# Performance work log

Measured on AMD Instinct MI355X. Metric: run time of the kernel, lower is better.

Reference implementation:

```python
import jax, jax.numpy as jnp
import numpy as np
import math

TAU = 0.04
BIG = 100000.0


def _decay(initial, step, steps):
    de = initial * 0.75 * (1.0 + math.cos(math.pi * step / (steps / 2.0)))
    dm = initial * 0.75 * (1.0 + math.cos(math.pi * step / steps))
    e = de if step < steps / 2.0 else 0.0
    m = dm
    return e, m, 3.0 - e - m


def _normalize(x):
    return x / jnp.maximum(jnp.linalg.norm(x, axis=1, keepdims=True), 1e-12)


def _pdist(a2, b2, ab):
    # ||a_i||^2 + ||b_j||^2 - 2 a_i.b_j, clamped + sqrt (matches torch addmm_ path)
    return jnp.sqrt(jnp.clip(a2 + b2.T - 2.0 * ab, 1e-12, None))


def _row_extreme(masked, is_min):
    idx = jnp.argmin(masked, axis=1) if is_min else jnp.argmax(masked, axis=1)
    val = jnp.take_along_axis(masked, idx[:, None], axis=1)[:, 0]
    return val, idx


def _nanmedian(vals, mask):
    # lower-median over valid entries per row (torch.nanmedian semantics)
    k = mask.sum(axis=1)
    pos = jnp.maximum((k - 1) // 2, 0)
    order = jnp.argsort(jnp.where(mask, vals, jnp.inf), axis=1)
    med_idx = jnp.take_along_axis(order, pos[:, None], axis=1)[:, 0]
    med_val = jnp.take_along_axis(vals, med_idx[:, None], axis=1)[:, 0]
    med_val = jnp.where(k > 0, med_val, 0.0)  # NaN-median -> 0 as in source
    return med_val, med_idx


def _ce0(logits):
    # CrossEntropy with labels all 0 over 2 classes
    return jnp.mean(jax.nn.logsumexp(logits, axis=1) - logits[:, 0])


def _pair_loss(dist_vals_an, dist_vals_ap, an_t, ap_t):
    sg = jax.lax.stop_gradient
    w_an = jnp.clip(sg(an_t) - sg(dist_vals_an), 0.0, None)
    w_ap = jnp.clip(sg(dist_vals_ap) - sg(ap_t), 0.0, None)
    logits = jnp.stack([w_an * dist_vals_an / TAU, w_ap * dist_vals_ap / TAU], axis=1)
    return _ce0(logits)


def _forward(teacher_inputs, inputs, epoch):
    e, m, d = _decay(0.5, epoch, 240)
    t = _normalize(teacher_inputs)
    s = _normalize(inputs)
    t2 = jnp.sum(t * t, axis=1, keepdims=True)  # [n,1]
    s2 = jnp.sum(s * s, axis=1, keepdims=True)
    dist_t = _pdist(t2, t2, t @ t.T)            # teacher-teacher [n,n]
    dist = _pdist(t2, s2, t @ s.T)              # teacher-student [n,n]
    temp1 = jnp.diag(dist)[:, None]             # dist[i,i] broadcast over row i
    neg_mask = dist_t > temp1
    pos_mask = ~neg_mask

    gather_t = lambda idx: jnp.take_along_axis(dist_t, idx[:, None], axis=1)[:, 0]

    # hard mining (d-branch): nearest negative, farthest positive
    an_v, an_i = _row_extreme(jnp.where(neg_mask, dist, BIG), True)
    ap_v, ap_i = _row_extreme(jnp.where(pos_mask, dist, 0.0), False)
    loss_d = _pair_loss(an_v, ap_v, gather_t(an_i), gather_t(ap_i))

    # easy mining (e-branch): farthest negative, nearest positive
    an_ev, an_ei = _row_extreme(jnp.where(neg_mask, dist, 0.0), False)
    ap_ev, ap_ei = _row_extreme(jnp.where(pos_mask, dist, BIG), True)
    loss_e = _pair_loss(an_ev, ap_ev, gather_t(an_ei), gather_t(ap_ei))

    # median mining (m-branch)
    an_mv, an_mi = _nanmedian(dist, neg_mask)
    ap_mv, ap_mi = _nanmedian(dist, pos_mask)
    loss_m = _pair_loss(an_mv, ap_mv, gather_t(an_mi), gather_t(ap_mi))

    return loss_e * e + loss_m * m + loss_d * d


def setup_inputs() -> dict:
    key = jax.random.key(0)
    k1, k2 = jax.random.split(key)
    n, dim = 4096, 2048
    return {
        "teacher_inputs": jax.random.normal(k1, (n, dim), dtype=jnp.float32),
        "inputs": jax.random.normal(k2, (n, dim), dtype=jnp.float32),
        "epoch": 100,
    }


def reference(teacher_inputs, inputs, epoch):
    return _forward(teacher_inputs, inputs, epoch)
```

## Files before the change

### kernel.cpp

```cpp
#include <hip/hip_runtime.h>
#include <math.h>
#include <cfloat>
#include <climits>

#define NROW 4096
#define DIM  2048
#define BIGF 100000.0f
#define BIGU 0x47C35000u

typedef float  f32x4  __attribute__((ext_vector_type(4)));
typedef __bf16 bf16x8 __attribute__((ext_vector_type(8)));
typedef unsigned short us8v __attribute__((ext_vector_type(8)));

__device__ __forceinline__ unsigned short f2bf(float x) {
    unsigned u = __float_as_uint(x);
    u += 0x7fffu + ((u >> 16) & 1u);
    return (unsigned short)(u >> 16);
}
__device__ __forceinline__ float bf2f(unsigned short h) {
    return __uint_as_float(((unsigned)h) << 16);
}

__device__ __forceinline__ void gload16(const void* g, void* lds) {
    __builtin_amdgcn_global_load_lds(
        (const __attribute__((address_space(1))) unsigned int*)g,
        (__attribute__((address_space(3))) unsigned int*)lds,
        16, 0, 0);
}

__global__ __launch_bounds__(256) void k_norm_split(const float* __restrict__ in,
    unsigned short* __restrict__ hi, unsigned short* __restrict__ lo,
    float* __restrict__ sq)
{
    int row = blockIdx.x;
    int tid = threadIdx.x;
    const float4* rp = (const float4*)(in + (size_t)row * DIM);
    float4 v0 = rp[tid * 2 + 0];
    float4 v1 = rp[tid * 2 + 1];
    float ss = v0.x*v0.x + v0.y*v0.y + v0.z*v0.z + v0.w*v0.w
             + v1.x*v1.x + v1.y*v1.y + v1.z*v1.z + v1.w*v1.w;
    #pragma unroll
    for (int off = 32; off > 0; off >>= 1) ss += __shfl_down(ss, off, 64);
    __shared__ float wsum[4];
    __shared__ float s_den;
    if ((tid & 63) == 0) wsum[tid >> 6] = ss;
    __syncthreads();
    if (tid == 0) {
        float tot = wsum[0] + wsum[1] + wsum[2] + wsum[3];
        float den = fmaxf(sqrtf(tot), 1e-12f);
        s_den = den;
        sq[row] = tot / (den * den);
    }
    __syncthreads();
    float den = s_den;
    float xs[8];
    xs[0]=v0.x/den; xs[1]=v0.y/den; xs[2]=v0.z/den; xs[3]=v0.w/den;
    xs[4]=v1.x/den; xs[5]=v1.y/den; xs[6]=v1.z/den; xs[7]=v1.w/den;
    us8v hv, lv;
    #pragma unroll
    for (int j = 0; j < 8; ++j) {
        unsigned short h = f2bf(xs[j]);
        hv[j] = h;
        lv[j] = f2bf(xs[j] - bf2f(h));
    }
    *(us8v*)&hi[(size_t)row * DIM + tid * 8] = hv;
    *(us8v*)&lo[(size_t)row * DIM + tid * 8] = lv;
}

__global__ __launch_bounds__(256, 2) void k_gemm_mfma(
    const unsigned short* __restrict__ T1, const unsigned short* __restrict__ T2,
    const unsigned short* __restrict__ S1, const unsigned short* __restrict__ S2,
    const float* __restrict__ t2v, const float* __restrict__ s2v,
    float* __restrict__ distT, float* __restrict__ distS)
{
    __shared__ unsigned short As[128 * 32];
    __shared__ unsigned short Bt[128 * 32];
    __shared__ unsigned short Bs[128 * 32];

    int tid = threadIdx.x;

    int orig  = blockIdx.y * gridDim.x + blockIdx.x;
    int nwg   = gridDim.x * gridDim.y;
    int cpx   = nwg >> 3;
    int swz   = (orig & 7) * cpx + (orig >> 3);
    int bx    = swz % gridDim.x;
    int by    = swz / gridDim.x;
    int m0 = by * 128, n0 = bx * 128;

    int r0   = tid >> 2;
    int cs0  = (((tid & 3) ^ ((r0 >> 1) & 3)) << 4);
    unsigned ldst = (unsigned)tid * 16;

    int l  = tid & 63;
    int w  = tid >> 6;
    int wr = w >> 1, wc = w & 1;
    int lr = l & 15;
    int kc = l >> 4;

    f32x4 acc_t[4][4], acc_s[4][4];
    #pragma unroll
    for (int m = 0; m < 4; ++m)
        #pragma unroll
        for (int n = 0; n < 4; ++n) {
            acc_t[m][n] = (f32x4)0.0f;
            acc_s[m][n] = (f32x4)0.0f;
        }

    const unsigned short* segA[3]  = {T1, T1, T2};
    const unsigned short* segBt[3] = {T1, T2, T1};
    const unsigned short* segBs[3] = {S1, S2, S1};

    for (int seg = 0; seg < 3; ++seg) {
        const char* pA  = (const char*)segA[seg];
        const char* pBt = (const char*)segBt[seg];
        const char* pBs = (const char*)segBs[seg];
        for (int k0 = 0; k0 < DIM; k0 += 32) {
            size_t gA0 = ((size_t)(m0 + r0)      * DIM + k0) * 2 + cs0;
            size_t gA1 = ((size_t)(m0 + 64 + r0) * DIM + k0) * 2 + cs0;
            size_t gB0 = ((size_t)(n0 + r0)      * DIM + k0) * 2 + cs0;
            size_t gB1 = ((size_t)(n0 + 64 + r0) * DIM + k0) * 2 + cs0;
            gload16(pA  + gA0, (char*)As + ldst);
            gload16(pA  + gA1, (char*)As + 4096 + ldst);
            gload16(pBt + gB0, (char*)Bt + ldst);
            gload16(pBt + gB1, (char*)Bt + 4096 + ldst);
            gload16(pBs + gB0, (char*)Bs + ldst);
            gload16(pBs + gB1, (char*)Bs + 4096 + ldst);
            __syncthreads();

            bf16x8 a[4], btf[4], bsf[4];
            #pragma unroll
            for (int m = 0; m < 4; ++m) {
                int ra = wr * 64 + m * 16 + lr;
                int co = ((kc ^ ((ra >> 1) & 3)) << 4);
                a[m] = *(const bf16x8*)((const char*)As + ra * 64 + co);
            }
            #pragma unroll
            for (int n = 0; n < 4; ++n) {
                int rb = wc * 64 + n * 16 + lr;
                int co = ((kc ^ ((rb >> 1) & 3)) << 4);
                btf[n] = *(const bf16x8*)((const char*)Bt + rb * 64 + co);
                bsf[n] = *(const bf16x8*)((const char*)Bs + rb * 64 + co);
            }
            #pragma unroll
            for (int m = 0; m < 4; ++m)
                #pragma unroll
                for (int n = 0; n < 4; ++n) {
                    acc_t[m][n] = __builtin_amdgcn_mfma_f32_16x16x32_bf16(
                        a[m], btf[n], acc_t[m][n], 0, 0, 0);
                    acc_s[m][n] = __builtin_amdgcn_mfma_f32_16x16x32_bf16(
                        a[m], bsf[n], acc_s[m][n], 0, 0, 0);
                }
            __syncthreads();
        }
    }

    int colb = n0 + wc * 64 + lr;
    int rowb = m0 + wr * 64 + (kc << 2);
    float t2row[4][4];
    #pragma unroll
    for (int m = 0; m < 4; ++m)
        #pragma unroll
        for (int r = 0; r < 4; ++r) t2row[m][r] = t2v[rowb + m * 16 + r];
    #pragma unroll
    for (int n = 0; n < 4; ++n) {
        int col = colb + n * 16;
        float t2c = t2v[col];
        float s2c = s2v[col];
        #pragma unroll
        for (int m = 0; m < 4; ++m) {
            f32x4 ct = acc_t[m][n];
            f32x4 cs = acc_s[m][n];
            int row = rowb + m * 16;
            #pragma unroll
            for (int r = 0; r < 4; ++r) {
                size_t o = (size_t)(row + r) * NROW + col;
                distT[o] = sqrtf(fmaxf(t2row[m][r] + t2c - 2.0f * ct[r], 1e-12f));
                distS[o] = sqrtf(fmaxf(t2row[m][r] + s2c - 2.0f * cs[r], 1e-12f));
            }
        }
    }
}

__device__ inline float pair_term(float an_v, float ap_v, float an_t, float ap_t)
{
    float w_an = fmaxf(an_t - an_v, 0.f);
    float w_ap = fmaxf(ap_v - ap_t, 0.f);
    float l0 = w_an * an_v / 0.04f;
    float l1 = w_ap * ap_v / 0.04f;
    float mx = fmaxf(l0, l1);
    return mx + logf(expf(l0 - mx) + expf(l1 - mx)) - l0;
}

__device__ __forceinline__ unsigned long long wred_min64(unsigned long long v) {
    #pragma unroll
    for (int o = 32; o > 0; o >>= 1) {
        unsigned long long x = __shfl_down(v, o, 64);
        v = (x < v) ? x : v;
    }
    return v;
}
__device__ __forceinline__ unsigned long long wred_max64(unsigned long long v) {
    #pragma unroll
    for (int o = 32; o > 0; o >>= 1) {
        unsigned long long x = __shfl_down(v, o, 64);
        v = (x > v) ? x : v;
    }
    return v;
}

__device__ void radix_select_reg(const unsigned u[16], unsigned negbits,
                                 unsigned selNeg, int rank,
                                 unsigned* hist, unsigned* s_wt, unsigned* s_sel,
                                 int tid, float& val, int& idx)
{
    unsigned prefix = 0;
    int r = rank;
    #pragma unroll
    for (int pass = 0; pass < 4; ++pass) {
        const int shift = 24 - pass * 8;
        hist[tid] = 0;
        __syncthreads();
        {
            unsigned curbin = 0xFFFFFFFFu, rl = 0;
            #pragma unroll
            for (int q = 0; q < 16; ++q) {
                unsigned key = (((negbits >> q) & 1u) == selNeg) ? u[q] : 0xFFFFFFFFu;
                bool match = (pass == 0) || ((key >> (shift + 8)) == (prefix >> (shift + 8)));
                if (match) {
                    unsigned b = (key >> shift) & 255u;
                    if (b == curbin) { rl++; }
                    else {
                        if (rl) atomicAdd(&hist[curbin], rl);
                        curbin = b; rl = 1;
                    }
                }
            }
            if (rl) atomicAdd(&hist[curbin], rl);
        }
        __syncthreads();
        unsigned h = hist[tid];
        unsigned incl = h;
        #pragma unroll
        for (int o = 1; o < 64; o <<= 1) {
            unsigned x = __shfl_up(incl, o, 64);
            if ((tid & 63) >= o) incl += x;
        }
        if ((tid & 63) == 63) s_wt[tid >> 6] = incl;
        __syncthreads();
        int wv = tid >> 6;
        unsigned base = 0;
        if (wv > 0) base += s_wt[0];
        if (wv > 1) base += s_wt[1];
        if (wv > 2) base += s_wt[2];
        incl += base;
        unsigned excl = incl - h;
        if ((unsigned)r >= excl && (unsigned)r < incl) {
            s_sel[0] = (unsigned)tid;
            s_sel[1] = (unsigned)r - excl;
        }
        __syncthreads();
        prefix |= s_sel[0] << shift;
        r = (int)s_sel[1];
        __syncthreads();
    }
    {
        unsigned cnt = 0;
        #pragma unroll
        for (int q = 0; q < 16; ++q) {
            unsigned key = (((negbits >> q) & 1u) == selNeg) ? u[q] : 0xFFFFFFFFu;
            if (key == prefix) cnt++;
        }
        hist[tid] = cnt;
        __syncthreads();
        unsigned incl = hist[tid];
        #pragma unroll
        for (int o = 1; o < 64; o <<= 1) {
            unsigned x = __shfl_up(incl, o, 64);
            if ((tid & 63) >= o) incl += x;
        }
        if ((tid & 63) == 63) s_wt[tid >> 6] = incl;
        __syncthreads();
        int wv = tid >> 6;
        unsigned base = 0;
        if (wv > 0) base += s_wt[0];
        if (wv > 1) base += s_wt[1];
        if (wv > 2) base += s_wt[2];
        incl += base;
        unsigned excl = incl - cnt;
        if ((unsigned)r >= excl && (unsigned)r < incl) {
            int need = r - (int)excl;
            #pragma unroll
            for (int q = 0; q < 16; ++q) {
                unsigned key = (((negbits >> q) & 1u) == selNeg) ? u[q] : 0xFFFFFFFFu;
                if (key == prefix) {
                    if (need == 0) { s_sel[0] = (unsigned)(tid * 16 + q); }
                    need--;
                }
            }
        }
        __syncthreads();
    }
    val = __uint_as_float(prefix);
    idx = (int)s_sel[0];
    __syncthreads();
}

__global__ __launch_bounds__(256) void k_rowstats(const float* __restrict__ distS,
    const float* __restrict__ distT, float* __restrict__ terms)
{
    __shared__ unsigned hist[256];
    __shared__ unsigned s_wt[4];
    __shared__ unsigned s_sel[2];
    __shared__ unsigned long long s_red[4][4];
    __shared__ int s_cw[4];
    __shared__ float s_t1;

    int i = blockIdx.x, tid = threadIdx.x;
    const float* dSrow = distS + (size_t)i * NROW;
    const float* dTrow = distT + (size_t)i * NROW;

    if (tid == 0) s_t1 = dSrow[i];

    float4 dv[4], tv[4];
    #pragma unroll
    for (int c = 0; c < 4; ++c) {
        dv[c] = *(const float4*)(dSrow + tid * 16 + c * 4);
        tv[c] = *(const float4*)(dTrow + tid * 16 + c * 4);
    }
    __syncthreads();
    float temp1 = s_t1;

    unsigned u[16];
    unsigned negbits = 0;
    #pragma unroll
    for (int c = 0; c < 4; ++c) {
        const float* dp = (const float*)&dv[c];
        const float* tp = (const float*)&tv[c];
        #pragma unroll
        for (int k = 0; k < 4; ++k) {
            int q = c * 4 + k;
            u[q] = __float_as_uint(dp[k]);
            if (tp[k] > temp1) negbits |= (1u << q);
        }
    }

    unsigned long long Pan  = ~0ull;
    unsigned long long Pap  = 0ull;
    unsigned long long Pane = 0ull;
    unsigned long long Pape = ~0ull;
    int cnt = 0;
    #pragma unroll
    for (int q = 0; q < 16; ++q) {
        unsigned j = (unsigned)(tid * 16 + q);
        unsigned neg = (negbits >> q) & 1u;
        cnt += (int)neg;
        unsigned kan  = neg ? u[q] : BIGU;
        unsigned kap  = neg ? 0u   : u[q];
        unsigned kane = neg ? u[q] : 0u;
        unsigned kape = neg ? BIGU : u[q];
        unsigned long long pan  = ((unsigned long long)kan  << 32) | j;
        unsigned long long pap  = ((unsigned long long)kap  << 32) | (0xFFFFFFFFu - j);
        unsigned long long pane = ((unsigned long long)kane << 32) | (0xFFFFFFFFu - j);
        unsigned long long pape = ((unsigned long long)kape << 32) | j;
        if (pan  < Pan)  Pan  = pan;
        if (pap  > Pap)  Pap  = pap;
        if (pane > Pane) Pane = pane;
        if (pape < Pape) Pape = pape;
    }
    Pan  = wred_min64(Pan);
    Pap  = wred_max64(Pap);
    Pane = wred_max64(Pane);
    Pape = wred_min64(Pape);
    #pragma unroll
    for (int o = 32; o > 0; o >>= 1) cnt += __shfl_down(cnt, o, 64);
    if ((tid & 63) == 0) {
        int wv = tid >> 6;
        s_red[0][wv] = Pan; s_red[1][wv] = Pap;
        s_red[2][wv] = Pane; s_red[3][wv] = Pape;
        s_cw[wv] = cnt;
    }
    __syncthreads();
    unsigned long long Ran = ~0ull, Rap = 0ull, Rane = 0ull, Rape = ~0ull;
    #pragma unroll
    for (int wv = 0; wv < 4; ++wv) {
        if (s_red[0][wv] < Ran)  Ran  = s_red[0][wv];
        if (s_red[1][wv] > Rap)  Rap  = s_red[1][wv];
        if (s_red[2][wv] > Rane) Rane = s_red[2][wv];
        if (s_red[3][wv] < Rape) Rape = s_red[3][wv];
    }
    int k_neg = s_cw[0] + s_cw[1] + s_cw[2] + s_cw[3];
    int k_pos = NROW - k_neg;

    float an_v  = __uint_as_float((unsigned)(Ran  >> 32)); int an_i  = (int)(Ran & 0xFFFFFFFFull);
    float ap_v  = __uint_as_float((unsigned)(Rap  >> 32)); int ap_i  = (int)(0xFFFFFFFFu - (unsigned)(Rap & 0xFFFFFFFFull));
    float ane_v = __uint_as_float((unsigned)(Rane >> 32)); int ane_i = (int)(0xFFFFFFFFu - (unsigned)(Rane & 0xFFFFFFFFull));
    float ape_v = __uint_as_float((unsigned)(Rape >> 32)); int ape_i = (int)(Rape & 0xFFFFFFFFull);

    __syncthreads();

    float mn_v; int mn_i;
    if (k_neg > 0) {
        radix_select_reg(u, negbits, 1u, (k_neg - 1) >> 1, hist, s_wt, s_sel, tid, mn_v, mn_i);
    } else { mn_v = 0.f; mn_i = 0; }
    float mp_v; int mp_i;
    if (k_pos > 0) {
        radix_select_reg(u, negbits, 0u, (k_pos - 1) >> 1, hist, s_wt, s_sel, tid, mp_v, mp_i);
    } else { mp_v = 0.f; mp_i = 0; }

    if (tid == 0) {
        float an_t  = dTrow[an_i];
        float ap_t  = dTrow[ap_i];
        float ane_t = dTrow[ane_i];
        float ape_t = dTrow[ape_i];
        float mn_t  = dTrow[mn_i];
        float mp_t  = dTrow[mp_i];
        terms[i]            = pair_term(an_v,  ap_v,  an_t,  ap_t);
        terms[NROW + i]     = pair_term(ane_v, ape_v, ane_t, ape_t);
        terms[2*NROW + i]   = pair_term(mn_v,  mp_v,  mn_t,  mp_t);
    }
}

__global__ __launch_bounds__(256) void k_finalize(const float* __restrict__ terms,
    const void* __restrict__ epoch_p, float* __restrict__ out)
{
    __shared__ float red[256];
    int tid = threadIdx.x;
    float s0 = 0.f, s1 = 0.f, s2 = 0.f;
    for (int j = tid; j < NROW; j += 256) {
        s0 += terms[j];
        s1 += terms[NROW + j];
        s2 += terms[2*NROW + j];
    }
    float tot[3];
    float sv[3] = {s0, s1, s2};
    for (int t = 0; t < 3; ++t) {
        red[tid] = sv[t];
        __syncthreads();
        for (int st = 128; st > 0; st >>= 1) {
            if (tid < st) red[tid] += red[tid + st];
            __syncthreads();
        }
        tot[t] = red[0];
        __syncthreads();
    }
    if (tid == 0) {
        int ei = *(const int*)epoch_p;
        double step;
        if (ei >= 0 && ei < 100000) step = (double)ei;
        else step = (double)(*(const float*)epoch_p);
        const double PI = 3.14159265358979323846;
        double de = 0.5 * 0.75 * (1.0 + cos(PI * step / 120.0));
        double dm = 0.5 * 0.75 * (1.0 + cos(PI * step / 240.0));
        double e = (step < 120.0) ? de : 0.0;
        double m = dm;
        double d = 3.0 - e - m;
        double loss_d = (double)tot[0] / (double)NROW;
        double loss_e = (double)tot[1] / (double)NROW;
        double loss_m = (double)tot[2] / (double)NROW;
        out[0] = (float)(loss_e * e + loss_m * m + loss_d * d);
    }
}

extern "C" void kernel_launch(void* const* d_in, const int* in_sizes, int n_in,
                              void* d_out, int out_size, void* d_ws, size_t ws_size,
                              hipStream_t stream)
{
    (void)in_sizes; (void)n_in; (void)out_size; (void)ws_size;
    const float* t_in = (const float*)d_in[0];
    const float* s_in = (const float*)d_in[1];
    const void*  epoch = d_in[2];
    float* out = (float*)d_out;

    char* ws = (char*)d_ws;
    size_t off = 0;
    unsigned short* T1 = (unsigned short*)(ws + off); off += (size_t)NROW * DIM * 2;
    unsigned short* T2 = (unsigned short*)(ws + off); off += (size_t)NROW * DIM * 2;
    unsigned short* S1 = (unsigned short*)(ws + off); off += (size_t)NROW * DIM * 2;
    unsigned short* S2 = (unsigned short*)(ws + off); off += (size_t)NROW * DIM * 2;
    float* t2v   = (float*)(ws + off); off += (size_t)NROW * 4;
    float* s2v   = (float*)(ws + off); off += (size_t)NROW * 4;
    float* distT = (float*)(ws + off); off += (size_t)NROW * NROW * 4;
    float* distS = (float*)(ws + off); off += (size_t)NROW * NROW * 4;
    float* terms = (float*)(ws + off); off += (size_t)3 * NROW * 4;

    k_norm_split<<<NROW, 256, 0, stream>>>(t_in, T1, T2, t2v);
    k_norm_split<<<NROW, 256, 0, stream>>>(s_in, S1, S2, s2v);
    k_gemm_mfma<<<dim3(32, 32), 256, 0, stream>>>(T1, T2, S1, S2, t2v, s2v, distT, distS);
    k_rowstats<<<NROW, 256, 0, stream>>>(distS, distT, terms);
    k_finalize<<<1, 256, 0, stream>>>(terms, epoch, out);
}
```

Before: 679.1 us.

## Double-buffer LDS tiles in fused bf16 MFMA distance GEMM

Replaces the single-buffered LDS staging with two 24KB buffers and flattens the three split-precision segments into one 192-step loop. The next tile's global-to-LDS loads are issued before the current tile's MFMAs, and one barrier per iteration replaces the previous two. This aims to hide global load latency behind compute. It doubles LDS use per block to 48KB, which may limit the two-blocks-per-CU occupancy target.

```diff
diff --git a/kernel.cpp b/kernel.cpp
--- a/kernel.cpp
+++ b/kernel.cpp
@@ -73,9 +73,7 @@
     const float* __restrict__ t2v, const float* __restrict__ s2v,
     float* __restrict__ distT, float* __restrict__ distS)
 {
-    __shared__ unsigned short As[128 * 32];
-    __shared__ unsigned short Bt[128 * 32];
-    __shared__ unsigned short Bs[128 * 32];
+    __shared__ __align__(16) unsigned char smem[2][24576];
 
     int tid = threadIdx.x;
 
@@ -106,52 +104,60 @@
             acc_s[m][n] = (f32x4)0.0f;
         }
 
-    const unsigned short* segA[3]  = {T1, T1, T2};
-    const unsigned short* segBt[3] = {T1, T2, T1};
-    const unsigned short* segBs[3] = {S1, S2, S1};
-
-    for (int seg = 0; seg < 3; ++seg) {
-        const char* pA  = (const char*)segA[seg];
-        const char* pBt = (const char*)segBt[seg];
-        const char* pBs = (const char*)segBs[seg];
-        for (int k0 = 0; k0 < DIM; k0 += 32) {
-            size_t gA0 = ((size_t)(m0 + r0)      * DIM + k0) * 2 + cs0;
-            size_t gA1 = ((size_t)(m0 + 64 + r0) * DIM + k0) * 2 + cs0;
-            size_t gB0 = ((size_t)(n0 + r0)      * DIM + k0) * 2 + cs0;
-            size_t gB1 = ((size_t)(n0 + 64 + r0) * DIM + k0) * 2 + cs0;
-            gload16(pA  + gA0, (char*)As + ldst);
-            gload16(pA  + gA1, (char*)As + 4096 + ldst);
-            gload16(pBt + gB0, (char*)Bt + ldst);
-            gload16(pBt + gB1, (char*)Bt + 4096 + ldst);
-            gload16(pBs + gB0, (char*)Bs + ldst);
-            gload16(pBs + gB1, (char*)Bs + 4096 + ldst);
-            __syncthreads();
-
-            bf16x8 a[4], btf[4], bsf[4];
-            #pragma unroll
-            for (int m = 0; m < 4; ++m) {
-                int ra = wr * 64 + m * 16 + lr;
-                int co = ((kc ^ ((ra >> 1) & 3)) << 4);
-                a[m] = *(const bf16x8*)((const char*)As + ra * 64 + co);
-            }
+    const int NT = 192;
+
+    auto stage = [&](int tt, unsigned char* base) {
+        int sg = tt >> 6;
+        int k0 = (tt & 63) << 5;
+        const char* pA  = (const char*)((sg == 2) ? T2 : T1);
+        const char* pBt = (const char*)((sg == 1) ? T2 : T1);
+        const char* pBs = (const char*)((sg == 1) ? S2 : S1);
+        size_t gA0 = ((size_t)(m0 + r0)      * DIM + k0) * 2 + cs0;
+        size_t gA1 = ((size_t)(m0 + 64 + r0) * DIM + k0) * 2 + cs0;
+        size_t gB0 = ((size_t)(n0 + r0)      * DIM + k0) * 2 + cs0;
+        size_t gB1 = ((size_t)(n0 + 64 + r0) * DIM + k0) * 2 + cs0;
+        gload16(pA  + gA0, base + ldst);
+        gload16(pA  + gA1, base + 4096  + ldst);
+        gload16(pBt + gB0, base + 8192  + ldst);
+        gload16(pBt + gB1, base + 12288 + ldst);
+        gload16(pBs + gB0, base + 16384 + ldst);
+        gload16(pBs + gB1, base + 20480 + ldst);
+    };
+
+    stage(0, smem[0]);
+    __syncthreads();
+
+    int cur = 0;
+    for (int t = 0; t < NT; ++t) {
+        if (t + 1 < NT) stage(t + 1, smem[cur ^ 1]);
+
+        const unsigned char* base = smem[cur];
+        bf16x8 a[4], btf[4], bsf[4];
+        #pragma unroll
+        for (int m = 0; m < 4; ++m) {
+            int ra = wr * 64 + m * 16 + lr;
+            int co = ((kc ^ ((ra >> 1) & 3)) << 4);
+            a[m] = *(const bf16x8*)(base + ra * 64 + co);
+        }
+        #pragma unroll
+        for (int n = 0; n < 4; ++n) {
+            int rb = wc * 64 + n * 16 + lr;
+            int co = ((kc ^ ((rb >> 1) & 3)) << 4);
+            btf[n] = *(const bf16x8*)(base + 8192  + rb * 64 + co);
+            bsf[n] = *(const bf16x8*)(base + 16384 + rb * 64 + co);
+        }
+        #pragma unroll
+        for (int m = 0; m < 4; ++m)
             #pragma unroll
             for (int n = 0; n < 4; ++n) {
-                int rb = wc * 64 + n * 16 + lr;
-                int co = ((kc ^ ((rb >> 1) & 3)) << 4);
-                btf[n] = *(const bf16x8*)((const char*)Bt + rb * 64 + co);
-                bsf[n] = *(const bf16x8*)((const char*)Bs + rb * 64 + co);
+                acc_t[m][n] = __builtin_amdgcn_mfma_f32_16x16x32_bf16(
+                    a[m], btf[n], acc_t[m][n], 0, 0, 0);
+                acc_s[m][n] = __builtin_amdgcn_mfma_f32_16x16x32_bf16(
+                    a[m], bsf[n], acc_s[m][n], 0, 0, 0);
             }
-            #pragma unroll
-            for (int m = 0; m < 4; ++m)
-                #pragma unroll
-                for (int n = 0; n < 4; ++n) {
-                    acc_t[m][n] = __builtin_amdgcn_mfma_f32_16x16x32_bf16(
-                        a[m], btf[n], acc_t[m][n], 0, 0, 0);
-                    acc_s[m][n] = __builtin_amdgcn_mfma_f32_16x16x32_bf16(
-                        a[m], bsf[n], acc_s[m][n], 0, 0, 0);
-                }
-            __syncthreads();
-        }
+
+        __syncthreads();
+        cur ^= 1;
     }
 
     int colb = n0 + wc * 64 + lr;
```

Result: no change. 668.6 us (-1.5%).

## Fuse split-bf16 GEMM segments per k-step with triple-buffered LDS prefetch

Applied to the files above, without the earlier changes.

The GEMM no longer runs three separate passes over K (hi*hi, hi*lo, lo*hi). Each k-step now loads the hi and lo tiles once and computes all three products from them, so the total number of tile loads and barriers per k drops from three passes to two stages. LDS grows from 24KB to 72KB as a triple buffer so the next tiles are prefetched while MFMA runs, which may reduce occupancy. The two normalize/split launches are also merged into a single grid.

```diff
diff --git a/kernel.cpp b/kernel.cpp
--- a/kernel.cpp
+++ b/kernel.cpp
@@ -28,11 +28,20 @@
         16, 0, 0);
 }
 
-__global__ __launch_bounds__(256) void k_norm_split(const float* __restrict__ in,
-    unsigned short* __restrict__ hi, unsigned short* __restrict__ lo,
-    float* __restrict__ sq)
-{
-    int row = blockIdx.x;
+__global__ __launch_bounds__(256) void k_norm_split(
+    const float* __restrict__ t_in, const float* __restrict__ s_in,
+    unsigned short* __restrict__ T1, unsigned short* __restrict__ T2,
+    unsigned short* __restrict__ S1, unsigned short* __restrict__ S2,
+    float* __restrict__ t2v, float* __restrict__ s2v)
+{
+    int b   = blockIdx.x;
+    int row = b & (NROW - 1);
+    bool isS = b >= NROW;
+    const float* in = isS ? s_in : t_in;
+    unsigned short* hi = isS ? S1 : T1;
+    unsigned short* lo = isS ? S2 : T2;
+    float* sq = isS ? s2v : t2v;
+
     int tid = threadIdx.x;
     const float4* rp = (const float4*)(in + (size_t)row * DIM);
     float4 v0 = rp[tid * 2 + 0];
@@ -73,9 +82,7 @@
     const float* __restrict__ t2v, const float* __restrict__ s2v,
     float* __restrict__ distT, float* __restrict__ distS)
 {
-    __shared__ unsigned short As[128 * 32];
-    __shared__ unsigned short Bt[128 * 32];
-    __shared__ unsigned short Bs[128 * 32];
+    __shared__ __align__(16) unsigned char smem[3][24576];
 
     int tid = threadIdx.x;
 
@@ -91,6 +98,11 @@
     int cs0  = (((tid & 3) ^ ((r0 >> 1) & 3)) << 4);
     unsigned ldst = (unsigned)tid * 16;
 
+    size_t offA0 = ((size_t)(m0 + r0)      * DIM) * 2 + cs0;
+    size_t offA1 = ((size_t)(m0 + 64 + r0) * DIM) * 2 + cs0;
+    size_t offB0 = ((size_t)(n0 + r0)      * DIM) * 2 + cs0;
+    size_t offB1 = ((size_t)(n0 + 64 + r0) * DIM) * 2 + cs0;
+
     int l  = tid & 63;
     int w  = tid >> 6;
     int wr = w >> 1, wc = w & 1;
@@ -106,52 +118,66 @@
             acc_s[m][n] = (f32x4)0.0f;
         }
 
-    const unsigned short* segA[3]  = {T1, T1, T2};
-    const unsigned short* segBt[3] = {T1, T2, T1};
-    const unsigned short* segBs[3] = {S1, S2, S1};
-
-    for (int seg = 0; seg < 3; ++seg) {
-        const char* pA  = (const char*)segA[seg];
-        const char* pBt = (const char*)segBt[seg];
-        const char* pBs = (const char*)segBs[seg];
-        for (int k0 = 0; k0 < DIM; k0 += 32) {
-            size_t gA0 = ((size_t)(m0 + r0)      * DIM + k0) * 2 + cs0;
-            size_t gA1 = ((size_t)(m0 + 64 + r0) * DIM + k0) * 2 + cs0;
-            size_t gB0 = ((size_t)(n0 + r0)      * DIM + k0) * 2 + cs0;
-            size_t gB1 = ((size_t)(n0 + 64 + r0) * DIM + k0) * 2 + cs0;
-            gload16(pA  + gA0, (char*)As + ldst);
-            gload16(pA  + gA1, (char*)As + 4096 + ldst);
-            gload16(pBt + gB0, (char*)Bt + ldst);
-            gload16(pBt + gB1, (char*)Bt + 4096 + ldst);
-            gload16(pBs + gB0, (char*)Bs + ldst);
-            gload16(pBs + gB1, (char*)Bs + 4096 + ldst);
-            __syncthreads();
-
-            bf16x8 a[4], btf[4], bsf[4];
-            #pragma unroll
-            for (int m = 0; m < 4; ++m) {
-                int ra = wr * 64 + m * 16 + lr;
-                int co = ((kc ^ ((ra >> 1) & 3)) << 4);
-                a[m] = *(const bf16x8*)((const char*)As + ra * 64 + co);
-            }
+    const char* cT1 = (const char*)T1;
+    const char* cT2 = (const char*)T2;
+    const char* cS1 = (const char*)S1;
+    const char* cS2 = (const char*)S2;
+
+    auto stage6 = [&](const char* sA, const char* sBt, const char* sBs,
+                      int kk, unsigned char* base) {
+        size_t kb = (size_t)kk << 6;
+        gload16(sA  + offA0 + kb, base + ldst);
+        gload16(sA  + offA1 + kb, base + 4096  + ldst);
+        gload16(sBt + offB0 + kb, base + 8192  + ldst);
+        gload16(sBt + offB1 + kb, base + 12288 + ldst);
+        gload16(sBs + offB0 + kb, base + 16384 + ldst);
+        gload16(sBs + offB1 + kb, base + 20480 + ldst);
+    };
+
+    auto compute_pair = [&](const unsigned char* aBase, const unsigned char* bBase) {
+        bf16x8 a[4], btf[4], bsf[4];
+        #pragma unroll
+        for (int m = 0; m < 4; ++m) {
+            int ra = wr * 64 + m * 16 + lr;
+            int co = ((kc ^ ((ra >> 1) & 3)) << 4);
+            a[m] = *(const bf16x8*)(aBase + ra * 64 + co);
+        }
+        #pragma unroll
+        for (int n = 0; n < 4; ++n) {
+            int rb = wc * 64 + n * 16 + lr;
+            int co = ((kc ^ ((rb >> 1) & 3)) << 4);
+            btf[n] = *(const bf16x8*)(bBase + 8192  + rb * 64 + co);
+            bsf[n] = *(const bf16x8*)(bBase + 16384 + rb * 64 + co);
+        }
+        #pragma unroll
+        for (int m = 0; m < 4; ++m)
             #pragma unroll
             for (int n = 0; n < 4; ++n) {
-                int rb = wc * 64 + n * 16 + lr;
-                int co = ((kc ^ ((rb >> 1) & 3)) << 4);
-                btf[n] = *(const bf16x8*)((const char*)Bt + rb * 64 + co);
-                bsf[n] = *(const bf16x8*)((const char*)Bs + rb * 64 + co);
+                acc_t[m][n] = __builtin_amdgcn_mfma_f32_16x16x32_bf16(
+                    a[m], btf[n], acc_t[m][n], 0, 0, 0);
+                acc_s[m][n] = __builtin_amdgcn_mfma_f32_16x16x32_bf16(
+                    a[m], bsf[n], acc_s[m][n], 0, 0, 0);
             }
-            #pragma unroll
-            for (int m = 0; m < 4; ++m)
-                #pragma unroll
-                for (int n = 0; n < 4; ++n) {
-                    acc_t[m][n] = __builtin_amdgcn_mfma_f32_16x16x32_bf16(
-                        a[m], btf[n], acc_t[m][n], 0, 0, 0);
-                    acc_s[m][n] = __builtin_amdgcn_mfma_f32_16x16x32_bf16(
-                        a[m], bsf[n], acc_s[m][n], 0, 0, 0);
-                }
-            __syncthreads();
-        }
+    };
+
+    unsigned char* pP = smem[0];
+    unsigned char* pQ = smem[1];
+    unsigned char* pN = smem[2];
+
+    stage6(cT1, cT1, cS1, 0, pP);
+    __syncthreads();
+
+    for (int k = 0; k < 64; ++k) {
+        stage6(cT2, cT2, cS2, k, pQ);
+        compute_pair(pP, pP);
+        __syncthreads();
+
+        if (k < 63) stage6(cT1, cT1, cS1, k + 1, pN);
+        compute_pair(pP, pQ);
+        compute_pair(pQ, pP);
+        __syncthreads();
+
+        unsigned char* t0 = pQ; pQ = pP; pP = pN; pN = t0;
     }
 
     int colb = n0 + wc * 64 + lr;
@@ -483,8 +509,7 @@
     float* distS = (float*)(ws + off); off += (size_t)NROW * NROW * 4;
     float* terms = (float*)(ws + off); off += (size_t)3 * NROW * 4;
 
-    k_norm_split<<<NROW, 256, 0, stream>>>(t_in, T1, T2, t2v);
-    k_norm_split<<<NROW, 256, 0, stream>>>(s_in, S1, S2, s2v);
+    k_norm_split<<<2 * NROW, 256, 0, stream>>>(t_in, s_in, T1, T2, S1, S2, t2v, s2v);
     k_gemm_mfma<<<dim3(32, 32), 256, 0, stream>>>(T1, T2, S1, S2, t2v, s2v, distT, distS);
     k_rowstats<<<NROW, 256, 0, stream>>>(distS, distT, terms);
     k_finalize<<<1, 256, 0, stream>>>(terms, epoch, out);
```

New measurement: 755.5 us. 1.11x slower.
